# Performance work log

Hardware: AMD Instinct MI355X
Metric: run time of the kernel (lower is better)

Reference implementation:

```python
import jax, jax.numpy as jnp
import numpy as np

P, A = 8, 65536            # poses, atoms per pose
N = P * A                  # total atoms
N1 = N + 1                 # kin nodes (node 0 = virtual root)


def _local_hts(dofs):
    """Per-node local homogeneous transform from bond DOFs.
    dofs[:,0]=phi (torsion), dofs[:,1]=theta (bond angle), dofs[:,2]=d (length).
    M = Rz(phi) @ Ry(theta) @ Trans_x(d)   (NeRF-style internal coordinates)."""
    phi, theta, d = dofs[:, 0], dofs[:, 1], dofs[:, 2]
    cp, sp = jnp.cos(phi), jnp.sin(phi)
    ct, st = jnp.cos(theta), jnp.sin(theta)
    z = jnp.zeros_like(phi)
    o = jnp.ones_like(phi)
    # R = Rz(phi) @ Ry(theta)
    r00, r01, r02 = cp * ct, -sp, cp * st
    r10, r11, r12 = sp * ct, cp, sp * st
    r20, r21, r22 = -st, z, ct
    # t = R @ [d,0,0]
    t0, t1, t2 = d * r00, d * r10, d * r20
    M = jnp.stack([
        jnp.stack([r00, r01, r02, t0], -1),
        jnp.stack([r10, r11, r12, t1], -1),
        jnp.stack([r20, r21, r22, t2], -1),
        jnp.stack([z, z, z, o], -1),
    ], -2)  # [N1,4,4]
    return M


def setup_inputs() -> dict:
    rng = np.random.default_rng(0)
    # tree: each node's parent is 1..4 nodes back (topologically sorted), root self-parented
    parents = np.zeros(N1, np.int32)
    idx = np.arange(1, N1)
    parents[1:] = np.maximum(idx - 1 - rng.integers(0, 4, size=N), 0).astype(np.int32)
    # kinforest.id: permutation mapping kin node (1..N) -> flat atom index
    kin_id = rng.permutation(N).astype(np.int32)
    # base DOFs (detached full_dofs): realistic bond geometry
    base = np.zeros((N1, 4), np.float32)
    base[:, 1] = rng.uniform(1.5, 2.2, N1)          # theta
    base[:, 2] = rng.normal(1.53, 0.02, N1)         # bond length
    masked = rng.uniform(-np.pi, np.pi, N1).astype(np.float32)  # torsion params
    bond_w = rng.uniform(0.5, 1.5, (P, A - 1)).astype(np.float32)
    pose_coords = np.zeros((P, A, 3), np.float32)
    return {
        "masked_dofs": jnp.asarray(masked),
        "base_dofs": jnp.asarray(base),
        "pose_coords": jnp.asarray(pose_coords),
        "bond_w": jnp.asarray(bond_w),
        "parents": jnp.asarray(parents),
        "kin_id": jnp.asarray(kin_id),
    }


def reference(masked_dofs, base_dofs, pose_coords, bond_w, parents, kin_id):
    # 1) write optimizable DOFs into full DOF tensor (dof_mask = torsion column)
    dofs = base_dofs.at[:, 0].set(masked_dofs)
    # 2) per-node local transforms; root = identity
    M = _local_hts(dofs)
    M = M.at[0].set(jnp.eye(4, dtype=M.dtype))
    # 3) forwardKin: compose parent->child transforms via pointer doubling
    n_iters = int(np.ceil(np.log2(N1)))
    def body(carry, _):
        G, p = carry
        G = jnp.einsum('nij,njk->nik', G[p], G)
        return (G, p[p]), None
    (G, _), _ = jax.lax.scan(body, (M, parents), None, length=n_iters)
    kincoords = G[1:, :3, 3]  # [N,3] global positions (skip root)
    # 4) scatter kin coords back into pose-stack coordinates
    flat = pose_coords.reshape(-1, 3).at[kin_id].set(kincoords)
    coords = flat.reshape(pose_coords.shape)  # [P,A,3]
    # 5) whole-pose scoring: weighted bonded quadratic energy per pose
    d = coords[:, 1:] - coords[:, :-1]
    energy = jnp.sum(bond_w * jnp.sum(d * d, -1), axis=-1)  # [P]
    return energy
```

## Files before the change

### kernel.cpp

```cpp
#include <hip/hip_runtime.h>

#define NN1    524289
#define PP     8
#define AA     65536
#define SEGLEN 64
#define NSEG   8193
#define CHUNK  33
#define NCHK   249
#define NE     (NCHK*4)

#define OFF_COORDS 0
#define OFF_NT   2097152
#define OFF_L1G  4194308
#define OFF_L1E  4587572
#define OFF_PREG 4620344
#define OFF_PREE 5013608
#define OFF_BCG  5046380
#define OFF_CLG  5058332
#define OFF_CLE  5070284

static __device__ __forceinline__ void set_ident(float* a){
  a[0]=1.f;a[1]=0.f;a[2]=0.f;a[3]=0.f;
  a[4]=0.f;a[5]=1.f;a[6]=0.f;a[7]=0.f;
  a[8]=0.f;a[9]=0.f;a[10]=1.f;a[11]=0.f;
}

static __device__ __forceinline__ void compose(const float* Aa, const float* B, float* O){
  #pragma unroll
  for(int r=0;r<3;r++){
    float a0=Aa[r*4+0],a1=Aa[r*4+1],a2=Aa[r*4+2],a3=Aa[r*4+3];
    O[r*4+0]=a0*B[0]+a1*B[4]+a2*B[8];
    O[r*4+1]=a0*B[1]+a1*B[5]+a2*B[9];
    O[r*4+2]=a0*B[2]+a1*B[6]+a2*B[10];
    O[r*4+3]=a0*B[3]+a1*B[7]+a2*B[11]+a3;
  }
}

static __device__ __forceinline__ void load12(const float4* b4, int idx, float* a){
  float4 x=b4[idx*3+0], y=b4[idx*3+1], z=b4[idx*3+2];
  a[0]=x.x;a[1]=x.y;a[2]=x.z;a[3]=x.w;
  a[4]=y.x;a[5]=y.y;a[6]=y.z;a[7]=y.w;
  a[8]=z.x;a[9]=z.y;a[10]=z.z;a[11]=z.w;
}
static __device__ __forceinline__ void store12(float4* b4, int idx, const float* a){
  b4[idx*3+0]=make_float4(a[0],a[1],a[2],a[3]);
  b4[idx*3+1]=make_float4(a[4],a[5],a[6],a[7]);
  b4[idx*3+2]=make_float4(a[8],a[9],a[10],a[11]);
}

static __device__ __forceinline__ void wave_scan(
    int w, int lane,
    const float* __restrict__ masked, const float4* __restrict__ base4,
    const int* __restrict__ parents,
    float G[12], int& pk)
{
  int i0 = w*SEGLEN;
  int i = i0 + lane;
  if(i == 0 || i >= NN1){
    set_ident(G); pk = 0xFF;
  } else {
    float4 b = base4[i];
    float phi = masked[i];
    float sp,cp,st,ct;
    __sincosf(phi,&sp,&cp);
    __sincosf(b.y,&st,&ct);
    float dd = b.z;
    G[0]=cp*ct; G[1]=-sp; G[2]=cp*st; G[3]=dd*G[0];
    G[4]=sp*ct; G[5]=cp;  G[6]=sp*st; G[7]=dd*G[4];
    G[8]=-st;   G[9]=0.f; G[10]=ct;   G[11]=dd*G[8];
    int rel = parents[i] - i0;
    pk = (rel >= 0) ? rel : (((rel+4)<<8) | 0xFF);
  }
  #pragma unroll
  for(int step=0; step<6; ++step){
    int ptr = pk & 0xFF;
    bool act = (ptr != 0xFF);
    int src = act ? ptr : lane;
    float g2[12];
    #pragma unroll
    for(int q=0;q<12;q++) g2[q] = __shfl(G[q], src, 64);
    int pk2 = __shfl(pk, src, 64);
    float ng[12];
    compose(g2, G, ng);
    #pragma unroll
    for(int q=0;q<12;q++) G[q] = act ? ng[q] : G[q];
    pk = act ? pk2 : pk;
  }
}

__global__ __launch_bounds__(1024) void fk1(
    const float* __restrict__ masked, const float4* __restrict__ base4,
    const int* __restrict__ parents,
    float4* __restrict__ L1G, int* __restrict__ L1E,
    float4* __restrict__ NT, float* __restrict__ out)
{
  if(blockIdx.x==0 && threadIdx.x < PP) out[threadIdx.x] = 0.f;
  int w = blockIdx.x*16 + (threadIdx.x>>6);
  if(w >= NSEG) return;
  int lane = threadIdx.x & 63;
  float G[12]; int pk;
  wave_scan(w, lane, masked, base4, parents, G, pk);
  int i = w*SEGLEN + lane;
  int tag = (pk>>8)&3;
  if(i < NN1){
    NT[i] = make_float4(G[3], G[7], G[11], __int_as_float(tag));
  }
  if(lane >= 60){
    int j = lane - 60;
    store12(L1G, w*4+j, G);
    L1E[w*4+j] = tag;
  }
}

__global__ __launch_bounds__(64) void fk2(
    const float4* __restrict__ L1G, const int* __restrict__ L1E,
    float4* __restrict__ PREG, int* __restrict__ PREE,
    float4* __restrict__ CLG, int* __restrict__ CLE)
{
  int g = blockIdx.x;
  int j = threadIdx.x;
  int s0 = g*CHUNK;
  int ns = min(CHUNK, NSEG - s0);
  int sj = s0 + min(j, ns-1);

  float A[4][12]; int at[4];
  #pragma unroll
  for(int t=0;t<4;t++){
    load12(L1G, sj*4+t, A[t]);
    at[t] = L1E[sj*4+t];
  }
  if(j >= ns){
    #pragma unroll
    for(int t=0;t<4;t++){ set_ident(A[t]); at[t]=t; }
  }

  #pragma unroll
  for(int step=0; step<6; ++step){
    int d = 1<<step;
    int src = (j >= d) ? (j - d) : j;
    float f[4][12]; int ft[4];
    #pragma unroll
    for(int t=0;t<4;t++){
      #pragma unroll
      for(int q=0;q<12;q++) f[t][q] = __shfl(A[t][q], src, 64);
      ft[t] = __shfl(at[t], src, 64);
    }
    bool act = (j >= d) && (j < ns);
    float nA[4][12]; int nt[4];
    #pragma unroll
    for(int t=0;t<4;t++){
      int tt = at[t];
      float sel[12];
      #pragma unroll
      for(int q=0;q<12;q++){
        float v01 = (tt&1) ? f[1][q] : f[0][q];
        float v23 = (tt&1) ? f[3][q] : f[2][q];
        sel[q] = (tt&2) ? v23 : v01;
      }
      compose(sel, A[t], nA[t]);
      int t01 = (tt&1) ? ft[1] : ft[0];
      int t23 = (tt&1) ? ft[3] : ft[2];
      nt[t] = (tt&2) ? t23 : t01;
    }
    #pragma unroll
    for(int t=0;t<4;t++){
      #pragma unroll
      for(int q=0;q<12;q++) A[t][q] = act ? nA[t][q] : A[t][q];
      at[t] = act ? nt[t] : at[t];
    }
  }

  if(j == 0){
    float I[12]; set_ident(I);
    #pragma unroll
    for(int t=0;t<4;t++){
      store12(PREG, s0*4+t, I);
      PREE[s0*4+t] = t;
    }
  }
  if(j < ns-1){
    #pragma unroll
    for(int t=0;t<4;t++){
      store12(PREG, (s0+j+1)*4+t, A[t]);
      PREE[(s0+j+1)*4+t] = at[t];
    }
  }
  if(j == ns-1){
    #pragma unroll
    for(int t=0;t<4;t++){
      store12(CLG, g*4+t, A[t]);
      CLE[g*4+t] = at[t];
    }
  }
}

__global__ __launch_bounds__(1024) void fk3(
    const float4* __restrict__ CLG, const int* __restrict__ CLE,
    float4* __restrict__ BCG)
{
  __shared__ float Lg[NE*12];
  __shared__ int   Le[NE];
  float4* Lg4 = (float4*)Lg;
  int tid = threadIdx.x;
  if(tid < NE){
    float a[12]; load12(CLG, tid, a);
    Lg4[tid*3+0]=make_float4(a[0],a[1],a[2],a[3]);
    Lg4[tid*3+1]=make_float4(a[4],a[5],a[6],a[7]);
    Lg4[tid*3+2]=make_float4(a[8],a[9],a[10],a[11]);
    Le[tid]=CLE[tid];
  }
  __syncthreads();
  for(int d=1; d<NCHK; d<<=1){
    float ng[12]; int ne2=0;
    bool doit = (tid<NE) && ((tid>>2)>=d);
    if(doit){
      int myE = Le[tid];
      int pe = ((tid>>2)-d)*4 + myE;
      float own[12], pg[12];
      load12(Lg4, tid, own);
      load12(Lg4, pe, pg);
      compose(pg, own, ng);
      ne2 = Le[pe];
    }
    __syncthreads();
    if(doit){
      Lg4[tid*3+0]=make_float4(ng[0],ng[1],ng[2],ng[3]);
      Lg4[tid*3+1]=make_float4(ng[4],ng[5],ng[6],ng[7]);
      Lg4[tid*3+2]=make_float4(ng[8],ng[9],ng[10],ng[11]);
      Le[tid]=ne2;
    }
    __syncthreads();
  }
  if(tid < NE){
    float b[12];
    if((tid>>2)==0){ set_ident(b); }
    else { load12(Lg4, tid-4, b); }
    store12(BCG, tid, b);
  }
}

__global__ __launch_bounds__(1024) void fk4(
    const int* __restrict__ kin, const float4* __restrict__ NT,
    const float4* __restrict__ PREG, const int* __restrict__ PREE,
    const float4* __restrict__ BCG,
    float4* __restrict__ coords)
{
  int w = blockIdx.x*16 + (threadIdx.x>>6);
  if(w >= NSEG) return;
  int lane = threadIdx.x & 63;
  int i = w*SEGLEN + lane;
  if(i == 0 || i >= NN1) return;
  float4 nt = NT[i];
  int tag = __float_as_int(nt.w) & 3;
  int c = w / CHUNK;
  int e = PREE[w*4+tag];
  float bg[12], pg[12], A[12];
  load12(BCG, c*4+e, bg);
  load12(PREG, w*4+tag, pg);
  compose(bg, pg, A);
  float x = A[0]*nt.x + A[1]*nt.y + A[2]*nt.z  + A[3];
  float y = A[4]*nt.x + A[5]*nt.y + A[6]*nt.z  + A[7];
  float z = A[8]*nt.x + A[9]*nt.y + A[10]*nt.z + A[11];
  coords[kin[i-1]] = make_float4(x, y, z, 0.f);
}

__global__ void fk5(const float4* __restrict__ coords, const float* __restrict__ bw,
                    float* __restrict__ out)
{
  int p = blockIdx.x >> 5;
  int sub = blockIdx.x & 31;
  int a0 = sub * 2048;
  int aend = min(a0 + 2048, AA - 1);
  float sum = 0.f;
  for(int a = a0 + (int)threadIdx.x; a < aend; a += 256){
    int r = p*AA + a;
    float4 c0 = coords[r], c1 = coords[r+1];
    float dx = c1.x-c0.x, dy = c1.y-c0.y, dz = c1.z-c0.z;
    sum += bw[p*(AA-1)+a]*(dx*dx+dy*dy+dz*dz);
  }
  #pragma unroll
  for(int off=32;off>0;off>>=1) sum += __shfl_down(sum, off, 64);
  __shared__ float red[4];
  int lane = threadIdx.x & 63, wid = threadIdx.x >> 6;
  if(lane==0) red[wid]=sum;
  __syncthreads();
  if(threadIdx.x==0){
    float tot = red[0]+red[1]+red[2]+red[3];
    atomicAdd(&out[p], tot);
  }
}

extern "C" void kernel_launch(void* const* d_in, const int* in_sizes, int n_in,
                              void* d_out, int out_size, void* d_ws, size_t ws_size,
                              hipStream_t stream)
{
  const float*  masked  = (const float*)d_in[0];
  const float4* base4   = (const float4*)d_in[1];
  const float*  bw      = (const float*)d_in[3];
  const int*    parents = (const int*)d_in[4];
  const int*    kin     = (const int*)d_in[5];

  float* ws = (float*)d_ws;
  float4* coords = (float4*)(ws + OFF_COORDS);
  float4* NT  = (float4*)(ws + OFF_NT);
  float4* L1G = (float4*)(ws + OFF_L1G);
  int*    L1E = (int*)(ws + OFF_L1E);
  float4* PREG= (float4*)(ws + OFF_PREG);
  int*    PREE= (int*)(ws + OFF_PREE);
  float4* BCG = (float4*)(ws + OFF_BCG);
  float4* CLG = (float4*)(ws + OFF_CLG);
  int*    CLE = (int*)(ws + OFF_CLE);
  float*  out = (float*)d_out;

  int nblk = (NSEG + 15) / 16;
  fk1<<<nblk, 1024, 0, stream>>>(masked, base4, parents, L1G, L1E, NT, out);
  fk2<<<NCHK, 64, 0, stream>>>(L1G, L1E, PREG, PREE, CLG, CLE);
  fk3<<<1, 1024, 0, stream>>>(CLG, CLE, BCG);
  fk4<<<nblk, 1024, 0, stream>>>(kin, NT, PREG, PREE, BCG, coords);
  fk5<<<PP*32, 256, 0, stream>>>(coords, bw, out);
}
```

Measured before the change: 50.38 us.

## Fuse coordinate scatter and bond energy via inverse kin permutation

Builds an inverse kin_id map in the first kernel, so the final stage can iterate in atom order and gather each atom's kin node instead of scattering coordinates. The coordinate-transform and energy-scoring kernels are merged. Positions now live in shared memory with overlapping 1023-atom tiles, which removes the coords buffer round trip and one launch. It also changes the chunk size from 33 to 64 segments, which alters the fk2/fk3 hierarchy. The cost is an extra random scatter write in fk1 and random gathers of NT, PREG and BCG.

```diff
diff --git a/kernel.cpp b/kernel.cpp
--- a/kernel.cpp
+++ b/kernel.cpp
@@ -1,23 +1,24 @@
 #include <hip/hip_runtime.h>
 
+#define N_TOT  524288
 #define NN1    524289
 #define PP     8
 #define AA     65536
 #define SEGLEN 64
 #define NSEG   8193
-#define CHUNK  33
-#define NCHK   249
+#define CHUNK  64
+#define NCHK   129
 #define NE     (NCHK*4)
 
-#define OFF_COORDS 0
-#define OFF_NT   2097152
-#define OFF_L1G  4194308
-#define OFF_L1E  4587572
-#define OFF_PREG 4620344
-#define OFF_PREE 5013608
-#define OFF_BCG  5046380
-#define OFF_CLG  5058332
-#define OFF_CLE  5070284
+#define OFF_NT    0
+#define OFF_KINV  2097156
+#define OFF_L1G   2621444
+#define OFF_L1E   3014708
+#define OFF_PREG  3047480
+#define OFF_PREE  3440744
+#define OFF_CLG   3473516
+#define OFF_CLE   3479708
+#define OFF_BCG   3480224
 
 static __device__ __forceinline__ void set_ident(float* a){
   a[0]=1.f;a[1]=0.f;a[2]=0.f;a[3]=0.f;
@@ -90,9 +91,10 @@
 
 __global__ __launch_bounds__(1024) void fk1(
     const float* __restrict__ masked, const float4* __restrict__ base4,
-    const int* __restrict__ parents,
+    const int* __restrict__ parents, const int* __restrict__ kin,
     float4* __restrict__ L1G, int* __restrict__ L1E,
-    float4* __restrict__ NT, float* __restrict__ out)
+    float4* __restrict__ NT, int* __restrict__ kinInv,
+    float* __restrict__ out)
 {
   if(blockIdx.x==0 && threadIdx.x < PP) out[threadIdx.x] = 0.f;
   int w = blockIdx.x*16 + (threadIdx.x>>6);
@@ -104,6 +106,7 @@
   int tag = (pk>>8)&3;
   if(i < NN1){
     NT[i] = make_float4(G[3], G[7], G[11], __int_as_float(tag));
+    if(i > 0) kinInv[kin[i-1]] = i;
   }
   if(lane >= 60){
     int j = lane - 60;
@@ -239,54 +242,58 @@
   }
 }
 
-__global__ __launch_bounds__(1024) void fk4(
-    const int* __restrict__ kin, const float4* __restrict__ NT,
+__global__ __launch_bounds__(1024) void fk45(
+    const int* __restrict__ kinInv, const float4* __restrict__ NT,
     const float4* __restrict__ PREG, const int* __restrict__ PREE,
-    const float4* __restrict__ BCG,
-    float4* __restrict__ coords)
-{
-  int w = blockIdx.x*16 + (threadIdx.x>>6);
-  if(w >= NSEG) return;
-  int lane = threadIdx.x & 63;
-  int i = w*SEGLEN + lane;
-  if(i == 0 || i >= NN1) return;
-  float4 nt = NT[i];
-  int tag = __float_as_int(nt.w) & 3;
-  int c = w / CHUNK;
-  int e = PREE[w*4+tag];
-  float bg[12], pg[12], A[12];
-  load12(BCG, c*4+e, bg);
-  load12(PREG, w*4+tag, pg);
-  compose(bg, pg, A);
-  float x = A[0]*nt.x + A[1]*nt.y + A[2]*nt.z  + A[3];
-  float y = A[4]*nt.x + A[5]*nt.y + A[6]*nt.z  + A[7];
-  float z = A[8]*nt.x + A[9]*nt.y + A[10]*nt.z + A[11];
-  coords[kin[i-1]] = make_float4(x, y, z, 0.f);
-}
-
-__global__ void fk5(const float4* __restrict__ coords, const float* __restrict__ bw,
-                    float* __restrict__ out)
-{
-  int p = blockIdx.x >> 5;
-  int sub = blockIdx.x & 31;
-  int a0 = sub * 2048;
-  int aend = min(a0 + 2048, AA - 1);
-  float sum = 0.f;
-  for(int a = a0 + (int)threadIdx.x; a < aend; a += 256){
-    int r = p*AA + a;
-    float4 c0 = coords[r], c1 = coords[r+1];
-    float dx = c1.x-c0.x, dy = c1.y-c0.y, dz = c1.z-c0.z;
-    sum += bw[p*(AA-1)+a]*(dx*dx+dy*dy+dz*dz);
-  }
-  #pragma unroll
-  for(int off=32;off>0;off>>=1) sum += __shfl_down(sum, off, 64);
-  __shared__ float red[4];
-  int lane = threadIdx.x & 63, wid = threadIdx.x >> 6;
-  if(lane==0) red[wid]=sum;
+    const float4* __restrict__ BCG, const float* __restrict__ bw,
+    float* __restrict__ out)
+{
+  __shared__ float spos[1024*3];
+  __shared__ float red0[16], red1[16];
+  int tid = threadIdx.x;
+  int base = blockIdx.x * 1023;
+  int r = base + tid;
+  if(r < N_TOT){
+    int i = kinInv[r];
+    float4 nt = NT[i];
+    int tag = __float_as_int(nt.w) & 3;
+    int w = i >> 6;
+    int c = w >> 6;
+    int e = PREE[w*4+tag];
+    float bg[12], pg[12], A[12];
+    load12(BCG, c*4+e, bg);
+    load12(PREG, w*4+tag, pg);
+    compose(bg, pg, A);
+    spos[tid*3+0] = A[0]*nt.x + A[1]*nt.y + A[2]*nt.z  + A[3];
+    spos[tid*3+1] = A[4]*nt.x + A[5]*nt.y + A[6]*nt.z  + A[7];
+    spos[tid*3+2] = A[8]*nt.x + A[9]*nt.y + A[10]*nt.z + A[11];
+  }
   __syncthreads();
-  if(threadIdx.x==0){
-    float tot = red[0]+red[1]+red[2]+red[3];
-    atomicAdd(&out[p], tot);
+  int pFirst = base >> 16;
+  float s0 = 0.f, s1 = 0.f;
+  if(tid < 1023 && r < N_TOT-1 && ((r & (AA-1)) != AA-1)){
+    float dx = spos[(tid+1)*3+0]-spos[tid*3+0];
+    float dy = spos[(tid+1)*3+1]-spos[tid*3+1];
+    float dz = spos[(tid+1)*3+2]-spos[tid*3+2];
+    int p = r >> 16;
+    int a = r & (AA-1);
+    float ev = bw[p*(AA-1)+a]*(dx*dx+dy*dy+dz*dz);
+    if(p == pFirst) s0 = ev; else s1 = ev;
+  }
+  #pragma unroll
+  for(int off=32; off>0; off>>=1){
+    s0 += __shfl_down(s0, off, 64);
+    s1 += __shfl_down(s1, off, 64);
+  }
+  int lane = tid & 63, wid = tid >> 6;
+  if(lane == 0){ red0[wid] = s0; red1[wid] = s1; }
+  __syncthreads();
+  if(tid == 0){
+    float t0 = 0.f, t1 = 0.f;
+    #pragma unroll
+    for(int q=0;q<16;q++){ t0 += red0[q]; t1 += red1[q]; }
+    atomicAdd(&out[pFirst], t0);
+    if(pFirst+1 < PP) atomicAdd(&out[pFirst+1], t1);
   }
 }
 
@@ -301,21 +308,21 @@
   const int*    kin     = (const int*)d_in[5];
 
   float* ws = (float*)d_ws;
-  float4* coords = (float4*)(ws + OFF_COORDS);
-  float4* NT  = (float4*)(ws + OFF_NT);
-  float4* L1G = (float4*)(ws + OFF_L1G);
-  int*    L1E = (int*)(ws + OFF_L1E);
-  float4* PREG= (float4*)(ws + OFF_PREG);
-  int*    PREE= (int*)(ws + OFF_PREE);
-  float4* BCG = (float4*)(ws + OFF_BCG);
-  float4* CLG = (float4*)(ws + OFF_CLG);
-  int*    CLE = (int*)(ws + OFF_CLE);
-  float*  out = (float*)d_out;
+  float4* NT   = (float4*)(ws + OFF_NT);
+  int*    kinInv = (int*)(ws + OFF_KINV);
+  float4* L1G  = (float4*)(ws + OFF_L1G);
+  int*    L1E  = (int*)(ws + OFF_L1E);
+  float4* PREG = (float4*)(ws + OFF_PREG);
+  int*    PREE = (int*)(ws + OFF_PREE);
+  float4* CLG  = (float4*)(ws + OFF_CLG);
+  int*    CLE  = (int*)(ws + OFF_CLE);
+  float4* BCG  = (float4*)(ws + OFF_BCG);
+  float*  out  = (float*)d_out;
 
   int nblk = (NSEG + 15) / 16;
-  fk1<<<nblk, 1024, 0, stream>>>(masked, base4, parents, L1G, L1E, NT, out);
+  int nblk45 = (N_TOT - 1 + 1022) / 1023;
+  fk1<<<nblk, 1024, 0, stream>>>(masked, base4, parents, kin, L1G, L1E, NT, kinInv, out);
   fk2<<<NCHK, 64, 0, stream>>>(L1G, L1E, PREG, PREE, CLG, CLE);
   fk3<<<1, 1024, 0, stream>>>(CLG, CLE, BCG);
-  fk4<<<nblk, 1024, 0, stream>>>(kin, NT, PREG, PREE, BCG, coords);
-  fk5<<<PP*32, 256, 0, stream>>>(coords, bw, out);
-}
+  fk45<<<nblk45, 1024, 0, stream>>>(kinInv, NT, PREG, PREE, BCG, bw, out);
+}
```

New measurement: 59.91 us. +18.9%, slower.
